# Performance work log

Measured on AMD Instinct MI355X. Metric: run time of the kernel, lower is better.

## Reference

```python
import jax, jax.numpy as jnp
import numpy as np

N = 131072          # number of items ranked in one soft_rank call
CAPACITY = 3.0      # self.capcity in the torch module


def _pav_kl(y, w):
    """KL isotonic regression (non-increasing fit) via Pool-Adjacent-Violators.
    Pooled block value = logsumexp(y_block) - logsumexp(w_block).
    Matches torchsort / fast-soft-sort isotonic_kl. Sequential O(N)."""
    n = y.shape[0]

    def push(i, st):
        ly, lw, val, start, ptr = st
        ly = ly.at[ptr].set(y[i])
        lw = lw.at[ptr].set(w[i])
        val = val.at[ptr].set(y[i] - w[i])
        start = start.at[ptr].set(i)
        ptr = ptr + 1

        def cond(s):
            _, _, v, _, p = s
            return (p >= 2) & (v[p - 2] <= v[p - 1])

        def merge(s):
            ly, lw, v, stt, p = s
            ny = jnp.logaddexp(ly[p - 2], ly[p - 1])
            nw = jnp.logaddexp(lw[p - 2], lw[p - 1])
            return (ly.at[p - 2].set(ny), lw.at[p - 2].set(nw),
                    v.at[p - 2].set(ny - nw), stt, p - 1)

        return jax.lax.while_loop(cond, merge, (ly, lw, val, start, ptr))

    z = jnp.zeros((n,), y.dtype)
    st0 = (z, z, z, jnp.full((n,), n, jnp.int32), jnp.int32(0))
    ly, lw, val, start, ptr = jax.lax.fori_loop(0, n, push, st0)
    # invalidate stale stack slots, then map each element to its block value
    start = jnp.where(jnp.arange(n) < ptr, start, n)
    blk = jnp.searchsorted(start, jnp.arange(n), side='right') - 1
    return val[blk]


@jax.custom_vjp
def isotonic_kl(y, w):
    return _pav_kl(y, w)


def _iso_fwd(y, w):
    sol = _pav_kl(y, w)
    return sol, (y, w, sol)


def _iso_bwd(res, g):
    y, w, sol = res
    n = y.shape[0]
    # blocks = maximal runs of constant solution (exact equality by construction)
    blk = jnp.cumsum(jnp.concatenate([jnp.array([True]), sol[1:] != sol[:-1]])) - 1
    gsum = jax.ops.segment_sum(g, blk, num_segments=n)

    def seg_softmax(v):
        m = jax.ops.segment_max(v, blk, num_segments=n)
        lse = jnp.log(jax.ops.segment_sum(jnp.exp(v - m[blk]), blk, num_segments=n)) + m
        return jnp.exp(v - lse[blk])

    return seg_softmax(y) * gsum[blk], -seg_softmax(w) * gsum[blk]


isotonic_kl.defvjp(_iso_fwd, _iso_bwd)


def soft_rank_kl(scores):
    """torchsort.soft_rank(scores[None], regularization='kl'), strength=1, ascending."""
    n = scores.shape[0]
    w_log = jnp.log(jnp.arange(n, 0, -1, dtype=scores.dtype))  # log([n, ..., 1])
    perm = jnp.argsort(-scores)          # descending, stable
    s = scores[perm]
    sol = isotonic_kl(s, w_log)
    inv = jnp.argsort(perm)
    return jnp.exp(s - sol)[inv]


def setup_inputs() -> dict:
    key = jax.random.key(0)
    k = jax.random.split(key, 5)
    x = jax.random.normal(k[0], (N, 1), jnp.float32)
    # torch Linear default init bounds: 1/sqrt(fan_in)
    w1 = jax.random.uniform(k[1], (1, 32), jnp.float32, -1.0, 1.0)
    b1 = jax.random.uniform(k[2], (32,), jnp.float32, -1.0, 1.0)
    lim2 = 1.0 / np.sqrt(32.0)
    w2 = jax.random.uniform(k[3], (32, 1), jnp.float32, -lim2, lim2)
    b2 = jax.random.uniform(k[4], (1,), jnp.float32, -lim2, lim2)
    return {"x": x, "w1": w1, "b1": b1, "w2": w2, "b2": b2}


def reference(x, w1, b1, w2, b2):
    h = jnp.maximum(x @ w1 + b1, 0.0)            # [N, 32]
    scores = (h @ w2 + b2).reshape(-1)           # [N]
    ranks = soft_rank_kl(scores)                 # [N]
    other = jax.lax.stop_gradient(ranks) % CAPACITY
    ranks = (ranks - other) / CAPACITY + 1.0
    return ranks.reshape(-1, 1)
```

## Files before the change

### kernel.cpp

```cpp
#include <hip/hip_runtime.h>
#include <stdint.h>

typedef unsigned int u32;
typedef unsigned long long u64;

#define N_ITEMS 131072
#define NB 131072
#define NSLICE 4
#define CHUNK 64
#define NCHUNKS 2048
#define SCAN_BLOCKS 512
#define FIXSCALE 268435456.0f
#define FIXMASK ((1ull << 46) - 1)


__device__ __forceinline__ float wsumf(int s, int e) {
  return 0.5f * (float)(e - s + 1) * (float)(2 * N_ITEMS - s - e);
}

__device__ __forceinline__ float key_to_score(u32 key) {
  u32 m = ~key;
  u32 u = (m & 0x80000000u) ? (m ^ 0x80000000u) : ~m;
  return __uint_as_float(u);
}

#define LOG2E 1.4426950408889634f
__device__ __forceinline__ float fexp(float x) { return exp2f(x * LOG2E); }

__device__ __forceinline__ u32 bucket_of(u32 key, u32 kmin, u32 kmax) {
  double scale = (double)NB / ((double)(kmax - kmin) + 1.0);
  u32 b = (u32)((double)(key - kmin) * scale);
  return b < NB ? b : (NB - 1);
}

__device__ __forceinline__ float recSY(int2 r) { return __int_as_float(r.y); }


__global__ void score_key_kernel(const float* __restrict__ x,
                                 const float* __restrict__ w1,
                                 const float* __restrict__ b1,
                                 const float* __restrict__ w2,
                                 const float* __restrict__ b2,
                                 u32* __restrict__ keyRaw,
                                 u32* __restrict__ pmin, u32* __restrict__ pmax,
                                 u64* __restrict__ hist8, u64* __restrict__ flags) {
  __shared__ u32 r0[256], r1[256];
  int t = threadIdx.x;
  int i = blockIdx.x * 256 + t;
#pragma unroll
  for (int k = 0; k < NSLICE; ++k) hist8[(size_t)k * NB + i] = 0ull;
  if (i < SCAN_BLOCKS) flags[i] = 0ull;
  float xv = x[i];
  float s = b2[0];
#pragma unroll
  for (int j = 0; j < 32; ++j) {
    float h = fmaf(xv, w1[j], b1[j]);
    h = fmaxf(h, 0.0f);
    s = fmaf(h, w2[j], s);
  }
  u32 u = __float_as_uint(s);
  u32 m = u ^ ((u & 0x80000000u) ? 0xFFFFFFFFu : 0x80000000u);
  u32 key = ~m;
  keyRaw[i] = key;
  r0[t] = key; r1[t] = key;
  __syncthreads();
  for (int off = 128; off > 0; off >>= 1) {
    if (t < off) { r0[t] = min(r0[t], r0[t + off]); r1[t] = max(r1[t], r1[t + off]); }
    __syncthreads();
  }
  if (t == 0) { pmin[blockIdx.x] = r0[0]; pmax[blockIdx.x] = r1[0]; }
}


__global__ void hist_kernel(const u32* __restrict__ keyRaw,
                            const u32* __restrict__ pmin, const u32* __restrict__ pmax,
                            u64* __restrict__ hist8, u32* __restrict__ mm) {
  __shared__ u32 s0[256], s1[256];
  int t = threadIdx.x;
  s0[t] = min(pmin[t], pmin[t + 256]);
  s1[t] = max(pmax[t], pmax[t + 256]);
  __syncthreads();
  for (int off = 128; off > 0; off >>= 1) {
    if (t < off) { s0[t] = min(s0[t], s0[t + off]); s1[t] = max(s1[t], s1[t + off]); }
    __syncthreads();
  }
  u32 kmin = s0[0], kmax = s1[0];
  if (blockIdx.x == 0 && t == 0) { mm[0] = kmin; mm[1] = kmax; }
  int i = blockIdx.x * 256 + t;
  u32 key = keyRaw[i];
  u32 g = bucket_of(key, kmin, kmax);
  float smax = key_to_score(kmin);
  float v = fexp(key_to_score(key) - smax);
  u64 fix = (u64)fmaxf(1.0f, fmaf(v, FIXSCALE, 0.5f));
  size_t slice = (size_t)(blockIdx.x & (NSLICE - 1)) * NB;
  atomicAdd(&hist8[slice + g], (1ull << 46) | fix);
}


__global__ __launch_bounds__(256) void scan_pav_kernel(const u64* __restrict__ hist8,
                                                       u64* __restrict__ flags,
                                                       u32* __restrict__ cdf,
                                                       u32* __restrict__ cstart,
                                                       int2* __restrict__ REC,
                                                       int* __restrict__ cnt) {
  __shared__ u32 sh[256];
  __shared__ float seL[256];
  __shared__ u32 cdfL[257];
  __shared__ u32 exclu_s;
  __shared__ u32 stkST[64][4];
  __shared__ float stkSY[64][4];
  int t = threadIdx.x, b = blockIdx.x;
  int i = b * 256 + t;
  u64 acc = 0;
#pragma unroll
  for (int c = 0; c < NSLICE; ++c) acc += hist8[(size_t)c * NB + i];
  u32 v = (u32)(acc >> 46);
  seL[t] = (float)(acc & FIXMASK) * (1.0f / FIXSCALE);
  sh[t] = v;
  __syncthreads();
  for (int off = 1; off < 256; off <<= 1) {
    u32 x2 = (t >= off) ? sh[t - off] : 0u;
    __syncthreads();
    sh[t] += x2;
    __syncthreads();
  }
  if (t == 0) {
    u32 agg = sh[255];
    if (b == 0) {
      atomicExch(&flags[0], (2ull << 32) | (u64)agg);
      exclu_s = 0u;
    } else {
      atomicExch(&flags[b], (1ull << 32) | (u64)agg);
      u32 ex = 0; int j = b - 1;
      for (;;) {
        u64 f = atomicAdd(&flags[j], 0ull);
        u32 st = (u32)(f >> 32);
        if (st == 0u) continue;
        ex += (u32)f;
        if (st == 2u) break;
        --j;
      }
      atomicExch(&flags[b], (2ull << 32) | (u64)(ex + agg));
      exclu_s = ex;
    }
  }
  __syncthreads();
  u32 exclu = exclu_s;
  u32 e = sh[t] - v + exclu;
  cdfL[t] = e;
  if (t == 255) cdfL[256] = exclu + sh[255];
  cdf[i] = e;
  if ((t & 63) == 0) cstart[i >> 6] = e;
  if (i == 0) cstart[NCHUNKS] = N_ITEMS;
  __syncthreads();
  if (t < 4) {
    int c = b * 4 + t;
    int ptr = 0; bool have = false;
    float syT = 0.0f; int stT = 0;
    for (int k = 0; k < 64; ++k) {
      u32 cs = cdfL[t * 64 + k], ce = cdfL[t * 64 + k + 1];
      if (ce == cs) continue;
      float syC = seL[t * 64 + k];
      int stC = (int)cs, eC = (int)ce - 1;
      while (have) {
        float SWc = wsumf(stC, eC);
        float SWt = wsumf(stT, stC - 1);
        if (!(syT * SWc <= syC * SWt)) break;
        syC += syT; stC = stT;
        if (ptr == 0) { have = false; break; }
        --ptr;
        stT = (int)stkST[ptr][t]; syT = stkSY[ptr][t];
      }
      if (have) { stkST[ptr][t] = (u32)stT; stkSY[ptr][t] = syT; ++ptr; }
      stT = stC; syT = syC; have = true;
    }
    int slotBase = c * 64;
    for (int k2 = 0; k2 < ptr; ++k2)
      REC[slotBase + k2] = make_int2((int)stkST[k2][t], __float_as_int(stkSY[k2][t]));
    int n = ptr;
    if (have) { REC[slotBase + n] = make_int2(stT, __float_as_int(syT)); ++n; }
    cnt[c] = n;
  }
}


__global__ void merge_multi_kernel(int2* __restrict__ REC,
                                   int* __restrict__ cnt, const u32* __restrict__ cstart,
                                   int l0, int L) {
  __shared__ int lcnt[64];
  __shared__ int ca[32], cb[32], cM[32];
  int t = threadIdx.x;
  int G = 1 << L;
  int SC = 1 << l0;
  int baseC = blockIdx.x * G * SC;
  if (t < G) lcnt[t] = cnt[baseC + t * SC];
  __syncthreads();
  for (int j = 0; j < L; ++j) {
    int P = G >> (j + 1);
    if (t < P) {
      int p = t;
      int kL = p << (j + 1), kR = kL + (1 << j);
      int slotL = (baseC + kL * SC) * 64, slotR = (baseC + kR * SC) * 64;
      int nL = lcnt[kL], nR = lcnt[kR];
      int a = 0, b = 0, hasM = 0;
      if (nL > 0 && nR > 0) {
        int gstartR = (int)cstart[baseC + kR * SC];
        int gendR   = (int)cstart[baseC + (kR + (1 << j)) * SC];
        int2 rL = REC[slotL + nL - 1];
        float SYL = recSY(rL); int stL = rL.x;
        int2 rR = REC[slotR];
        float SYR = recSY(rR);
        int eR = (nR > 1) ? (REC[slotR + 1].x - 1) : (gendR - 1);
        float SWL = wsumf(stL, gstartR - 1);
        float SWR = wsumf(gstartR, eR);
        if (SYL * SWR <= SYR * SWL) {
          hasM = 1;
          float SYM = SYL + SYR; int Ms = stL, Me = eR;
          a = 1; b = 1;
          for (;;) {
            float SWM = wsumf(Ms, Me);
            if (a < nL) {
              int2 re = REC[slotL + nL - 1 - a];
              float SYe = recSY(re); int ste = re.x;
              float SWe = wsumf(ste, Ms - 1);
              if (SYe * SWM <= SYM * SWe) { SYM += SYe; Ms = ste; ++a; continue; }
            }
            if (b < nR) {
              int2 rb = REC[slotR + b];
              float SYb = recSY(rb); int sb = rb.x;
              int eb = (b + 1 < nR) ? (REC[slotR + b + 1].x - 1) : (gendR - 1);
              float SWb = wsumf(sb, eb);
              if (SYM * SWb <= SYb * SWM) { SYM += SYb; Me = eb; ++b; continue; }
            }
            break;
          }
          REC[slotL + nL - a] = make_int2(Ms, __float_as_int(SYM));
        }
      }
      ca[p] = a; cb[p] = b; cM[p] = hasM;
    }
    __syncthreads();
    for (int p = 0; p < P; ++p) {
      int kL = p << (j + 1), kR = kL + (1 << j);
      int nL = lcnt[kL], nR = lcnt[kR];
      int a = ca[p], b = cb[p], hasM = cM[p];
      int slotL = (baseC + kL * SC) * 64, slotR = (baseC + kR * SC) * 64;
      int destBase = slotL + nL - a + hasM;
      int srcBase = slotR + b;
      int ncopy = nR - b;
      for (int off = 0; off < ncopy; off += blockDim.x) {
        int k2 = off + t; bool act = k2 < ncopy;
        int2 vr = make_int2(0, 0);
        if (act) vr = REC[srcBase + k2];
        __syncthreads();
        if (act) REC[destBase + k2] = vr;
        __syncthreads();
      }
    }
    __syncthreads();
    if (t < P) {
      int p = t; int kL = p << (j + 1), kR = kL + (1 << j);
      lcnt[kL] = lcnt[kL] - ca[p] + cM[p] + (lcnt[kR] - cb[p]);
    }
    __syncthreads();
  }
  if (t == 0) cnt[baseC] = lcnt[0];
}


__global__ void out_kernel(const u32* __restrict__ keyRaw, const u32* __restrict__ mm,
                           const u32* __restrict__ cdf,
                           const int2* __restrict__ REC,
                           const int* __restrict__ cnt, float* __restrict__ out) {
  int i = blockIdx.x * 256 + threadIdx.x;
  u32 key = keyRaw[i];
  u32 kmin = mm[0], kmax = mm[1];
  float smax = key_to_score(kmin);
  u32 g = bucket_of(key, kmin, kmax);
  int p = (int)cdf[g];
  int m = cnt[0];
  int lo = 0, hi = m - 1;
  while (lo < hi) {
    int mid = (lo + hi + 1) >> 1;
    if (REC[mid].x <= p) lo = mid; else hi = mid - 1;
  }
  int2 r = REC[lo];
  int s0 = r.x;
  int e0 = (lo + 1 < m) ? (REC[lo + 1].x - 1) : (N_ITEMS - 1);
  float SW = wsumf(s0, e0);
  float s = key_to_score(key);
  float rank = fexp(s - smax) * SW / recSY(r);
  out[i] = floorf(rank * (1.0f / 3.0f)) + 1.0f;
}


extern "C" void kernel_launch(void* const* d_in, const int* in_sizes, int n_in,
                              void* d_out, int out_size, void* d_ws, size_t ws_size,
                              hipStream_t stream) {
  const float* x  = (const float*)d_in[0];
  const float* w1 = (const float*)d_in[1];
  const float* b1 = (const float*)d_in[2];
  const float* w2 = (const float*)d_in[3];
  const float* b2 = (const float*)d_in[4];
  float* out = (float*)d_out;

  char* ws = (char*)d_ws;
  size_t o = 0;
  u32* mm     = (u32*)(ws + o); o += 16;
  u32* pmin   = (u32*)(ws + o); o += (size_t)SCAN_BLOCKS * 4;
  u32* pmax   = (u32*)(ws + o); o += (size_t)SCAN_BLOCKS * 4;
  u64* hist8  = (u64*)(ws + o); o += (size_t)NSLICE * NB * 8;
  u64* flags  = (u64*)(ws + o); o += (size_t)SCAN_BLOCKS * 8;
  u32* cdf    = (u32*)(ws + o); o += (size_t)(NB + 4) * 4;
  u32* cstart = (u32*)(ws + o); o += (size_t)(NCHUNKS + 4) * 4;
  u32* keyRaw = (u32*)(ws + o); o += (size_t)N_ITEMS * 4;
  int2* REC   = (int2*)(ws + o); o += (size_t)N_ITEMS * 8;
  int* cnt    = (int*)(ws + o);  o += (size_t)NCHUNKS * 4;

  score_key_kernel<<<SCAN_BLOCKS, 256, 0, stream>>>(x, w1, b1, w2, b2,
                                                    keyRaw, pmin, pmax, hist8, flags);
  hist_kernel<<<SCAN_BLOCKS, 256, 0, stream>>>(keyRaw, pmin, pmax, hist8, mm);
  scan_pav_kernel<<<SCAN_BLOCKS, 256, 0, stream>>>(hist8, flags, cdf, cstart, REC, cnt);
  merge_multi_kernel<<<64, 256, 0, stream>>>(REC, cnt, cstart, 0, 5);
  merge_multi_kernel<<<8, 256, 0, stream>>>(REC, cnt, cstart, 5, 3);
  merge_multi_kernel<<<1, 1024, 0, stream>>>(REC, cnt, cstart, 8, 3);
  out_kernel<<<SCAN_BLOCKS, 256, 0, stream>>>(keyRaw, mm, cdf, REC, cnt, out);
}
```

Before: 133.2 us.

## Fuse scan, per-chunk PAV and first merge levels into one shared-memory kernel

The scan kernel now runs with 64 blocks that each own 2048 buckets. Inside each block it does the decoupled-lookback prefix scan, runs PAV on 32 chunks, and merges those chunks through five levels in shared memory before writing one region's blocks to global memory. This removes one merge launch and the global-memory round trips of the per-chunk records in the first merge stage. In exchange the scan uses 8x fewer blocks, the serial lookback chain is shorter but each block does more serial work, and shared-memory use per block goes up, which lowers parallelism.

Result: faster. 117.5 us (-11.8%).

```diff
diff --git a/kernel.cpp b/kernel.cpp
--- a/kernel.cpp
+++ b/kernel.cpp
@@ -7,9 +7,12 @@
 #define N_ITEMS 131072
 #define NB 131072
 #define NSLICE 4
-#define CHUNK 64
 #define NCHUNKS 2048
-#define SCAN_BLOCKS 512
+#define MBLK 64
+#define BUCK_PER_BLK 2048
+#define CH_PER_BLK 32
+#define PAD 65
+#define REGSLOT 2048
 #define FIXSCALE 268435456.0f
 #define FIXMASK ((1ull << 46) - 1)
 
@@ -49,7 +52,7 @@
   int i = blockIdx.x * 256 + t;
 #pragma unroll
   for (int k = 0; k < NSLICE; ++k) hist8[(size_t)k * NB + i] = 0ull;
-  if (i < SCAN_BLOCKS) flags[i] = 0ull;
+  if (i < MBLK) flags[i] = 0ull;
   float xv = x[i];
   float s = b2[0];
 #pragma unroll
@@ -97,26 +100,32 @@
 }
 
 
-__global__ __launch_bounds__(256) void scan_pav_kernel(const u64* __restrict__ hist8,
-                                                       u64* __restrict__ flags,
-                                                       u32* __restrict__ cdf,
-                                                       u32* __restrict__ cstart,
-                                                       int2* __restrict__ REC,
-                                                       int* __restrict__ cnt) {
+__global__ __launch_bounds__(256) void scan_pav_merge_kernel(
+    const u64* __restrict__ hist8, u64* __restrict__ flags,
+    u32* __restrict__ cdf, int2* __restrict__ REC,
+    int* __restrict__ cnt2, u32* __restrict__ rstart) {
+  __shared__ u32 vals[BUCK_PER_BLK + 1];
+  __shared__ float seL[BUCK_PER_BLK];
+  __shared__ int   rST[CH_PER_BLK * PAD];
+  __shared__ float rSY[CH_PER_BLK * PAD];
   __shared__ u32 sh[256];
-  __shared__ float seL[256];
-  __shared__ u32 cdfL[257];
   __shared__ u32 exclu_s;
-  __shared__ u32 stkST[64][4];
-  __shared__ float stkSY[64][4];
+  __shared__ int lcnt[CH_PER_BLK];
+  __shared__ int ca[16], cb[16], cM[16];
   int t = threadIdx.x, b = blockIdx.x;
-  int i = b * 256 + t;
-  u64 acc = 0;
+  int B0 = b * BUCK_PER_BLK;
+  for (int q = 0; q < 8; ++q) {
+    int ii = q * 256 + t;
+    u64 acc = 0;
 #pragma unroll
-  for (int c = 0; c < NSLICE; ++c) acc += hist8[(size_t)c * NB + i];
-  u32 v = (u32)(acc >> 46);
-  seL[t] = (float)(acc & FIXMASK) * (1.0f / FIXSCALE);
-  sh[t] = v;
+    for (int c = 0; c < NSLICE; ++c) acc += hist8[(size_t)c * NB + B0 + ii];
+    vals[ii] = (u32)(acc >> 46);
+    seL[ii] = (float)(acc & FIXMASK) * (1.0f / FIXSCALE);
+  }
+  __syncthreads();
+  u32 loc[8]; u32 s = 0;
+  for (int q = 0; q < 8; ++q) { loc[q] = s; s += vals[t * 8 + q]; }
+  sh[t] = s;
   __syncthreads();
   for (int off = 1; off < 256; off <<= 1) {
     u32 x2 = (t >= off) ? sh[t - off] : 0u;
@@ -133,7 +142,7 @@
       atomicExch(&flags[b], (1ull << 32) | (u64)agg);
       u32 ex = 0; int j = b - 1;
       for (;;) {
-        u64 f = atomicAdd(&flags[j], 0ull);
+        u64 f = atomicAdd((u64*)&flags[j], 0ull);
         u32 st = (u32)(f >> 32);
         if (st == 0u) continue;
         ex += (u32)f;
@@ -146,19 +155,24 @@
   }
   __syncthreads();
   u32 exclu = exclu_s;
-  u32 e = sh[t] - v + exclu;
-  cdfL[t] = e;
-  if (t == 255) cdfL[256] = exclu + sh[255];
-  cdf[i] = e;
-  if ((t & 63) == 0) cstart[i >> 6] = e;
-  if (i == 0) cstart[NCHUNKS] = N_ITEMS;
-  __syncthreads();
-  if (t < 4) {
-    int c = b * 4 + t;
+  u32 tbase = ((t == 0) ? 0u : sh[t - 1]) + exclu;
+  u32 eb8[8];
+  for (int q = 0; q < 8; ++q) { eb8[q] = tbase + loc[q]; vals[t * 8 + q] = eb8[q]; }
+  {
+    uint4* c4 = (uint4*)(cdf + B0 + t * 8);
+    c4[0] = make_uint4(eb8[0], eb8[1], eb8[2], eb8[3]);
+    c4[1] = make_uint4(eb8[4], eb8[5], eb8[6], eb8[7]);
+  }
+  if (t == 255) vals[BUCK_PER_BLK] = exclu + sh[255];
+  if (t == 0) rstart[b] = exclu;
+  if (b == 0 && t == 0) rstart[MBLK] = N_ITEMS;
+  __syncthreads();
+  if (t < CH_PER_BLK) {
+    int base = t * PAD;
     int ptr = 0; bool have = false;
     float syT = 0.0f; int stT = 0;
     for (int k = 0; k < 64; ++k) {
-      u32 cs = cdfL[t * 64 + k], ce = cdfL[t * 64 + k + 1];
+      u32 cs = vals[t * 64 + k], ce = vals[t * 64 + k + 1];
       if (ce == cs) continue;
       float syC = seL[t * 64 + k];
       int stC = (int)cs, eC = (int)ce - 1;
@@ -169,43 +183,108 @@
         syC += syT; stC = stT;
         if (ptr == 0) { have = false; break; }
         --ptr;
-        stT = (int)stkST[ptr][t]; syT = stkSY[ptr][t];
-      }
-      if (have) { stkST[ptr][t] = (u32)stT; stkSY[ptr][t] = syT; ++ptr; }
+        stT = rST[base + ptr]; syT = rSY[base + ptr];
+      }
+      if (have) { rST[base + ptr] = stT; rSY[base + ptr] = syT; ++ptr; }
       stT = stC; syT = syC; have = true;
     }
-    int slotBase = c * 64;
-    for (int k2 = 0; k2 < ptr; ++k2)
-      REC[slotBase + k2] = make_int2((int)stkST[k2][t], __float_as_int(stkSY[k2][t]));
-    int n = ptr;
-    if (have) { REC[slotBase + n] = make_int2(stT, __float_as_int(syT)); ++n; }
-    cnt[c] = n;
-  }
-}
-
-
-__global__ void merge_multi_kernel(int2* __restrict__ REC,
-                                   int* __restrict__ cnt, const u32* __restrict__ cstart,
-                                   int l0, int L) {
-  __shared__ int lcnt[64];
-  __shared__ int ca[32], cb[32], cM[32];
+    if (have) { rST[base + ptr] = stT; rSY[base + ptr] = syT; ++ptr; }
+    lcnt[t] = ptr;
+  }
+  __syncthreads();
+  for (int j = 0; j < 5; ++j) {
+    int P = CH_PER_BLK >> (j + 1);
+    if (t < P) {
+      int p = t;
+      int kL = p << (j + 1), kR = kL + (1 << j);
+      int slotL = kL * PAD, slotR = kR * PAD;
+      int nL = lcnt[kL], nR = lcnt[kR];
+      int a = 0, bb = 0, hasM = 0;
+      if (nL > 0 && nR > 0) {
+        int gstartR = (int)vals[kR * 64];
+        int gendR   = (int)vals[(kR + (1 << j)) * 64];
+        float SYL = rSY[slotL + nL - 1]; int stL = rST[slotL + nL - 1];
+        float SYR = rSY[slotR];
+        int eR = (nR > 1) ? (rST[slotR + 1] - 1) : (gendR - 1);
+        float SWL = wsumf(stL, gstartR - 1);
+        float SWR = wsumf(gstartR, eR);
+        if (SYL * SWR <= SYR * SWL) {
+          hasM = 1;
+          float SYM = SYL + SYR; int Ms = stL, Me = eR;
+          a = 1; bb = 1;
+          for (;;) {
+            float SWM = wsumf(Ms, Me);
+            if (a < nL) {
+              float SYe = rSY[slotL + nL - 1 - a]; int ste = rST[slotL + nL - 1 - a];
+              float SWe = wsumf(ste, Ms - 1);
+              if (SYe * SWM <= SYM * SWe) { SYM += SYe; Ms = ste; ++a; continue; }
+            }
+            if (bb < nR) {
+              float SYb = rSY[slotR + bb]; int sb = rST[slotR + bb];
+              int eb = (bb + 1 < nR) ? (rST[slotR + bb + 1] - 1) : (gendR - 1);
+              float SWb = wsumf(sb, eb);
+              if (SYM * SWb <= SYb * SWM) { SYM += SYb; Me = eb; ++bb; continue; }
+            }
+            break;
+          }
+          rST[slotL + nL - a] = Ms; rSY[slotL + nL - a] = SYM;
+        }
+      }
+      ca[p] = a; cb[p] = bb; cM[p] = hasM;
+    }
+    __syncthreads();
+    for (int p = 0; p < P; ++p) {
+      int kL = p << (j + 1), kR = kL + (1 << j);
+      int nL = lcnt[kL], nR = lcnt[kR];
+      int a = ca[p], bb = cb[p], hasM = cM[p];
+      int slotL = kL * PAD, slotR = kR * PAD;
+      int destBase = slotL + nL - a + hasM;
+      int srcBase = slotR + bb;
+      int ncopy = nR - bb;
+      for (int off = 0; off < ncopy; off += blockDim.x) {
+        int k2 = off + t; bool act = k2 < ncopy;
+        int vt = 0; float vs = 0.f;
+        if (act) { vt = rST[srcBase + k2]; vs = rSY[srcBase + k2]; }
+        __syncthreads();
+        if (act) { rST[destBase + k2] = vt; rSY[destBase + k2] = vs; }
+        __syncthreads();
+      }
+    }
+    __syncthreads();
+    if (t < P) {
+      int p = t; int kL = p << (j + 1), kR = kL + (1 << j);
+      lcnt[kL] = lcnt[kL] - ca[p] + cM[p] + (lcnt[kR] - cb[p]);
+    }
+    __syncthreads();
+  }
+  int n = lcnt[0];
+  for (int k = t; k < n; k += blockDim.x)
+    REC[(size_t)b * REGSLOT + k] = make_int2(rST[k], __float_as_int(rSY[k]));
+  if (t == 0) cnt2[b] = n;
+}
+
+
+__global__ void merge_region_kernel(int2* __restrict__ REC, int* __restrict__ cnt2,
+                                    const u32* __restrict__ rstart, int l0, int L) {
+  __shared__ int lcnt[8];
+  __shared__ int ca[4], cb[4], cM[4];
   int t = threadIdx.x;
   int G = 1 << L;
-  int SC = 1 << l0;
-  int baseC = blockIdx.x * G * SC;
-  if (t < G) lcnt[t] = cnt[baseC + t * SC];
+  int SR = 1 << l0;
+  int baseR = blockIdx.x * G * SR;
+  if (t < G) lcnt[t] = cnt2[baseR + t * SR];
   __syncthreads();
   for (int j = 0; j < L; ++j) {
     int P = G >> (j + 1);
     if (t < P) {
       int p = t;
       int kL = p << (j + 1), kR = kL + (1 << j);
-      int slotL = (baseC + kL * SC) * 64, slotR = (baseC + kR * SC) * 64;
+      int slotL = (baseR + kL * SR) * REGSLOT, slotR = (baseR + kR * SR) * REGSLOT;
       int nL = lcnt[kL], nR = lcnt[kR];
-      int a = 0, b = 0, hasM = 0;
+      int a = 0, bb = 0, hasM = 0;
       if (nL > 0 && nR > 0) {
-        int gstartR = (int)cstart[baseC + kR * SC];
-        int gendR   = (int)cstart[baseC + (kR + (1 << j)) * SC];
+        int gstartR = (int)rstart[baseR + kR * SR];
+        int gendR   = (int)rstart[baseR + (kR + (1 << j)) * SR];
         int2 rL = REC[slotL + nL - 1];
         float SYL = recSY(rL); int stL = rL.x;
         int2 rR = REC[slotR];
@@ -216,7 +295,7 @@
         if (SYL * SWR <= SYR * SWL) {
           hasM = 1;
           float SYM = SYL + SYR; int Ms = stL, Me = eR;
-          a = 1; b = 1;
+          a = 1; bb = 1;
           for (;;) {
             float SWM = wsumf(Ms, Me);
             if (a < nL) {
@@ -225,29 +304,29 @@
               float SWe = wsumf(ste, Ms - 1);
               if (SYe * SWM <= SYM * SWe) { SYM += SYe; Ms = ste; ++a; continue; }
             }
-            if (b < nR) {
-              int2 rb = REC[slotR + b];
+            if (bb < nR) {
+              int2 rb = REC[slotR + bb];
               float SYb = recSY(rb); int sb = rb.x;
-              int eb = (b + 1 < nR) ? (REC[slotR + b + 1].x - 1) : (gendR - 1);
+              int eb = (bb + 1 < nR) ? (REC[slotR + bb + 1].x - 1) : (gendR - 1);
               float SWb = wsumf(sb, eb);
-              if (SYM * SWb <= SYb * SWM) { SYM += SYb; Me = eb; ++b; continue; }
+              if (SYM * SWb <= SYb * SWM) { SYM += SYb; Me = eb; ++bb; continue; }
             }
             break;
           }
           REC[slotL + nL - a] = make_int2(Ms, __float_as_int(SYM));
         }
       }
-      ca[p] = a; cb[p] = b; cM[p] = hasM;
+      ca[p] = a; cb[p] = bb; cM[p] = hasM;
     }
     __syncthreads();
     for (int p = 0; p < P; ++p) {
       int kL = p << (j + 1), kR = kL + (1 << j);
       int nL = lcnt[kL], nR = lcnt[kR];
-      int a = ca[p], b = cb[p], hasM = cM[p];
-      int slotL = (baseC + kL * SC) * 64, slotR = (baseC + kR * SC) * 64;
+      int a = ca[p], bb = cb[p], hasM = cM[p];
+      int slotL = (baseR + kL * SR) * REGSLOT, slotR = (baseR + kR * SR) * REGSLOT;
       int destBase = slotL + nL - a + hasM;
-      int srcBase = slotR + b;
-      int ncopy = nR - b;
+      int srcBase = slotR + bb;
+      int ncopy = nR - bb;
       for (int off = 0; off < ncopy; off += blockDim.x) {
         int k2 = off + t; bool act = k2 < ncopy;
         int2 vr = make_int2(0, 0);
@@ -264,21 +343,21 @@
     }
     __syncthreads();
   }
-  if (t == 0) cnt[baseC] = lcnt[0];
+  if (t == 0) cnt2[baseR] = lcnt[0];
 }
 
 
 __global__ void out_kernel(const u32* __restrict__ keyRaw, const u32* __restrict__ mm,
                            const u32* __restrict__ cdf,
                            const int2* __restrict__ REC,
-                           const int* __restrict__ cnt, float* __restrict__ out) {
+                           const int* __restrict__ cnt2, float* __restrict__ out) {
   int i = blockIdx.x * 256 + threadIdx.x;
   u32 key = keyRaw[i];
   u32 kmin = mm[0], kmax = mm[1];
   float smax = key_to_score(kmin);
   u32 g = bucket_of(key, kmin, kmax);
   int p = (int)cdf[g];
-  int m = cnt[0];
+  int m = cnt2[0];
   int lo = 0, hi = m - 1;
   while (lo < hi) {
     int mid = (lo + hi + 1) >> 1;
@@ -307,22 +386,21 @@
   char* ws = (char*)d_ws;
   size_t o = 0;
   u32* mm     = (u32*)(ws + o); o += 16;
-  u32* pmin   = (u32*)(ws + o); o += (size_t)SCAN_BLOCKS * 4;
-  u32* pmax   = (u32*)(ws + o); o += (size_t)SCAN_BLOCKS * 4;
+  u32* pmin   = (u32*)(ws + o); o += (size_t)512 * 4;
+  u32* pmax   = (u32*)(ws + o); o += (size_t)512 * 4;
   u64* hist8  = (u64*)(ws + o); o += (size_t)NSLICE * NB * 8;
-  u64* flags  = (u64*)(ws + o); o += (size_t)SCAN_BLOCKS * 8;
+  u64* flags  = (u64*)(ws + o); o += (size_t)MBLK * 8;
   u32* cdf    = (u32*)(ws + o); o += (size_t)(NB + 4) * 4;
-  u32* cstart = (u32*)(ws + o); o += (size_t)(NCHUNKS + 4) * 4;
+  u32* rstart = (u32*)(ws + o); o += (size_t)(MBLK + 4) * 4;
   u32* keyRaw = (u32*)(ws + o); o += (size_t)N_ITEMS * 4;
   int2* REC   = (int2*)(ws + o); o += (size_t)N_ITEMS * 8;
-  int* cnt    = (int*)(ws + o);  o += (size_t)NCHUNKS * 4;
-
-  score_key_kernel<<<SCAN_BLOCKS, 256, 0, stream>>>(x, w1, b1, w2, b2,
-                                                    keyRaw, pmin, pmax, hist8, flags);
-  hist_kernel<<<SCAN_BLOCKS, 256, 0, stream>>>(keyRaw, pmin, pmax, hist8, mm);
-  scan_pav_kernel<<<SCAN_BLOCKS, 256, 0, stream>>>(hist8, flags, cdf, cstart, REC, cnt);
-  merge_multi_kernel<<<64, 256, 0, stream>>>(REC, cnt, cstart, 0, 5);
-  merge_multi_kernel<<<8, 256, 0, stream>>>(REC, cnt, cstart, 5, 3);
-  merge_multi_kernel<<<1, 1024, 0, stream>>>(REC, cnt, cstart, 8, 3);
-  out_kernel<<<SCAN_BLOCKS, 256, 0, stream>>>(keyRaw, mm, cdf, REC, cnt, out);
-}
+  int* cnt2   = (int*)(ws + o);  o += (size_t)MBLK * 4;
+
+  score_key_kernel<<<512, 256, 0, stream>>>(x, w1, b1, w2, b2,
+                                            keyRaw, pmin, pmax, hist8, flags);
+  hist_kernel<<<512, 256, 0, stream>>>(keyRaw, pmin, pmax, hist8, mm);
+  scan_pav_merge_kernel<<<MBLK, 256, 0, stream>>>(hist8, flags, cdf, REC, cnt2, rstart);
+  merge_region_kernel<<<8, 256, 0, stream>>>(REC, cnt2, rstart, 0, 3);
+  merge_region_kernel<<<1, 1024, 0, stream>>>(REC, cnt2, rstart, 3, 3);
+  out_kernel<<<512, 256, 0, stream>>>(keyRaw, mm, cdf, REC, cnt2, out);
+}
```
